# Performance work log

Measured on AMD Instinct MI355X. Metric: run time of the kernel, lower is better.

Reference implementation:

```python
import jax, jax.numpy as jnp
import numpy as np

B, S, DIM = 16, 1024, 1024
GAMMA = 0.96875
EPS = 1e-3  # keras GroupNormalization default epsilon


def setup_inputs() -> dict:
    key = jax.random.key(0)
    ks = jax.random.split(key, 4)
    scale = 1.0 / np.sqrt(DIM)
    return {
        "x": jax.random.normal(ks[0], (B, S, DIM), dtype=jnp.float32),
        "Wq": jax.random.normal(ks[1], (DIM, DIM), dtype=jnp.float32) * scale,
        "Wk": jax.random.normal(ks[2], (DIM, DIM), dtype=jnp.float32) * scale,
        "Wv": jax.random.normal(ks[3], (DIM, DIM), dtype=jnp.float32) * scale,
        "gn_scale": jnp.ones((DIM,), dtype=jnp.float32),
        "gn_beta": jnp.zeros((DIM,), dtype=jnp.float32),
    }


def reference(x, Wq, Wk, Wv, gn_scale, gn_beta):
    # Bias-free projections
    Q = x @ Wq  # [B,S,D]
    K = x @ Wk
    V = x @ Wv
    # Full (non-causal) exponential decay matrix D[i,j] = gamma^(i-j)
    idx = jnp.arange(S, dtype=jnp.float32)
    D = GAMMA ** (idx[:, None] - idx[None, :])  # [S,S]
    scores = jnp.einsum("bsd,btd->bst", Q, K) * D  # [B,S,S]
    y = scores @ V  # [B,S,D]
    # GroupNorm with groups == channels: normalize each channel over seq axis
    mean = jnp.mean(y, axis=1, keepdims=True)  # [B,1,D]
    var = jnp.var(y, axis=1, keepdims=True)
    y_hat = (y - mean) * jax.lax.rsqrt(var + EPS)
    return y_hat * gn_scale + gn_beta
```

## Files before the change

### kernel.cpp

```cpp
#include <hip/hip_runtime.h>
#include <cmath>

#define BATCH_ 16
#define SN_ 1024
#define DN_ 1024

constexpr float EPS_ = 1e-3f;

typedef unsigned short ushort;
typedef __attribute__((ext_vector_type(8))) short short8;
typedef __attribute__((ext_vector_type(8))) unsigned short ushort8;
typedef __attribute__((ext_vector_type(16))) float f32x16;

__device__ __forceinline__ ushort f2b(float f) {
    unsigned u = __float_as_uint(f);
    unsigned r = (u + 0x7fffu + ((u >> 16) & 1u)) >> 16;
    return (ushort)r;
}

__device__ __forceinline__ void gload16(const void* g, void* l) {
    __builtin_amdgcn_global_load_lds(
        (const __attribute__((address_space(1))) void*)g,
        (__attribute__((address_space(3))) void*)l, 16, 0, 0);
}

template<int MODE>
__global__ __launch_bounds__(512, 2)
void gemm_bf(const ushort* __restrict__ A0, const ushort* __restrict__ B0,
             void* __restrict__ C0, long sA, long sB, long sBm, long sC,
             float coef)
{
    constexpr bool TRANSP = (MODE == 2 || MODE == 3);
    constexpr bool SCALE  = (MODE == 1 || MODE == 3);

    __shared__ __align__(16) char lds[131072];

    const int gx = gridDim.x, gy = gridDim.y;
    int lid   = blockIdx.x + gx * (blockIdx.y + gy * blockIdx.z);
    int total = gx * gy * gridDim.z;
    int swz   = (lid & 7) * (total >> 3) + (lid >> 3);
    int bx = swz % gx;
    int rest = swz / gx;
    int by = rest % gy;
    int bz = rest / gy;

    const int m0 = by * 256, n0 = bx * 256;
    const ushort* A  = A0 + (long)bz * sA;
    const ushort* Bp = B0 + (long)bz * sB + (long)(m0 >> 10) * sBm;

    const int t = threadIdx.x;
    const int l = t & 63, w = t >> 6;
    const int wr = w >> 2, wc = w & 3;
    const int ln = l & 31;
    const int kb = l >> 5;
    const int lx = l & 7;

    const int aOff = (wr * 128 + ln) * 128;
    const int bOff = 32768 + (wc * 64 + ln) * 128;

    const int rl   = t >> 3;
    const int slot = (t & 7) ^ (rl & 7);
    const ushort* gA = A  + (long)(m0 + rl) * 1024 + slot * 8;
    const ushort* gB = Bp + (long)(n0 + rl) * 1024 + slot * 8;
    char* lA = lds + t * 16;
    char* lB = lds + 32768 + t * 16;

    f32x16 acc[4][2] = {};

#pragma unroll
    for (int h = 0; h < 4; ++h) {
        gload16(gA + (long)h * 64 * 1024, lA + h * 8192);
        gload16(gB + (long)h * 64 * 1024, lB + h * 8192);
    }
    __syncthreads();

    int buf = 0;
    for (int kt = 0; kt < 16; ++kt) {
        if (kt < 15) {
            int k0 = (kt + 1) * 64;
            int bo = (buf ^ 1) * 65536;
#pragma unroll
            for (int h = 0; h < 4; ++h) {
                gload16(gA + (long)h * 64 * 1024 + k0, lA + bo + h * 8192);
                gload16(gB + (long)h * 64 * 1024 + k0, lB + bo + h * 8192);
            }
        }
        const int bo = buf * 65536;
#pragma unroll
        for (int ks = 0; ks < 4; ++ks) {
            const int sx = ((ks * 2 + kb) ^ lx) * 16;
            short8 av[4], bv[2];
#pragma unroll
            for (int mi = 0; mi < 4; ++mi)
                av[mi] = *(const short8*)(lds + bo + aOff + mi * 4096 + sx);
#pragma unroll
            for (int nj = 0; nj < 2; ++nj)
                bv[nj] = *(const short8*)(lds + bo + bOff + nj * 4096 + sx);
            __builtin_amdgcn_s_setprio(1);
#pragma unroll
            for (int mi = 0; mi < 4; ++mi)
#pragma unroll
                for (int nj = 0; nj < 2; ++nj)
                    acc[mi][nj] = __builtin_amdgcn_mfma_f32_32x32x16_bf16(
                        av[mi], bv[nj], acc[mi][nj], 0, 0, 0);
            __builtin_amdgcn_s_setprio(0);
        }
        __syncthreads();
        buf ^= 1;
    }

    if constexpr (MODE == 0) {
        float* C = (float*)C0 + (long)bz * sC;
#pragma unroll
        for (int mi = 0; mi < 4; ++mi)
#pragma unroll
            for (int reg = 0; reg < 16; ++reg) {
                int row = m0 + wr * 128 + mi * 32 + (reg & 3) + 8 * (reg >> 2) + 4 * kb;
#pragma unroll
                for (int nj = 0; nj < 2; ++nj)
                    C[(long)row * 1024 + n0 + wc * 64 + nj * 32 + ln] =
                        acc[mi][nj][reg];
            }
    } else if constexpr (!TRANSP) {
        ushort* C = (ushort*)C0 + (long)bz * sC;
#pragma unroll
        for (int mi = 0; mi < 4; ++mi)
#pragma unroll
            for (int reg = 0; reg < 16; ++reg) {
                int row = m0 + wr * 128 + mi * 32 + (reg & 3) + 8 * (reg >> 2) + 4 * kb;
                float s = SCALE ? exp2f(coef * (float)(row & 1023)) : 1.0f;
#pragma unroll
                for (int nj = 0; nj < 2; ++nj)
                    C[(long)row * 1024 + n0 + wc * 64 + nj * 32 + ln] =
                        f2b(acc[mi][nj][reg] * s);
            }
    } else {
        ushort* Tl = (ushort*)lds;
        const int bb = m0 >> 10;
        const int ms = m0 & 1023;
        ushort* Ct = (ushort*)C0 + (long)bb * sC;
#pragma unroll
        for (int mi = 0; mi < 4; ++mi)
#pragma unroll
            for (int reg = 0; reg < 16; ++reg) {
                int rm = wr * 128 + mi * 32 + (reg & 3) + 8 * (reg >> 2) + 4 * kb;
                float s = SCALE ? exp2f(coef * (float)(ms + rm)) : 1.0f;
#pragma unroll
                for (int nj = 0; nj < 2; ++nj) {
                    int cn = wc * 64 + nj * 32 + ln;
                    int p  = (rm >> 3) ^ (cn & 31);
                    Tl[cn * 256 + p * 8 + (rm & 7)] = f2b(acc[mi][nj][reg] * s);
                }
            }
        __syncthreads();
#pragma unroll
        for (int it = 0; it < 16; ++it) {
            int cn = (t >> 5) + it * 16;
            int ch = t & 31;
            int p  = ch ^ (cn & 31);
            ushort8 v = *(const ushort8*)&Tl[cn * 256 + p * 8];
            *(ushort8*)&Ct[(long)(n0 + cn) * 1024 + ms + ch * 8] = v;
        }
    }
}

__global__ __launch_bounds__(256)
void conv_x_k(const float* __restrict__ x, ushort* __restrict__ xb)
{
    long i = ((long)blockIdx.x * 256 + threadIdx.x) * 8;
    float4 a = *(const float4*)&x[i];
    float4 b = *(const float4*)&x[i + 4];
    ushort8 v;
    v[0] = f2b(a.x); v[1] = f2b(a.y); v[2] = f2b(a.z); v[3] = f2b(a.w);
    v[4] = f2b(b.x); v[5] = f2b(b.y); v[6] = f2b(b.z); v[7] = f2b(b.w);
    *(ushort8*)&xb[i] = v;
}

__global__ __launch_bounds__(256)
void wt_k(const float* __restrict__ W, ushort* __restrict__ Wt)
{
    __shared__ float Tl[32][33];
    int tx = threadIdx.x & 31, ty = threadIdx.x >> 5;
    int c0 = blockIdx.x * 32, r0 = blockIdx.y * 32;
#pragma unroll
    for (int i = 0; i < 4; i++)
        Tl[ty + 8 * i][tx] = W[(long)(r0 + ty + 8 * i) * 1024 + c0 + tx];
    __syncthreads();
#pragma unroll
    for (int i = 0; i < 4; i++)
        Wt[(long)(c0 + ty + 8 * i) * 1024 + r0 + tx] = f2b(Tl[tx][ty + 8 * i]);
}

__global__ __launch_bounds__(256)
void stats1(const float* __restrict__ y, float* __restrict__ psum,
            float* __restrict__ psumsq)
{
    int d = blockIdx.x * 256 + threadIdx.x;
    int b = blockIdx.y;
    int z = blockIdx.z;
    const float* p = y + ((long)b * SN_ + (long)z * 128) * DN_ + d;
    float s = 0.f, ss = 0.f;
    for (int i = 0; i < 128; i++) {
        float v = p[(long)i * DN_];
        s += v;
        ss += v * v;
    }
    long o = ((long)z * BATCH_ + b) * DN_ + d;
    psum[o] = s;
    psumsq[o] = ss;
}

__global__ __launch_bounds__(256)
void stats2(const float* __restrict__ psum, const float* __restrict__ psumsq,
            const float* __restrict__ gsc, const float* __restrict__ gbt,
            float* __restrict__ fs, float* __restrict__ bias)
{
    int d = blockIdx.x * 256 + threadIdx.x;
    int b = blockIdx.y;
    float s = 0.f, ss = 0.f;
    for (int z = 0; z < 8; z++) {
        long o = ((long)z * BATCH_ + b) * DN_ + d;
        s += psum[o];
        ss += psumsq[o];
    }
    float mean = s * (1.0f / SN_);
    float var  = ss * (1.0f / SN_) - mean * mean;
    var = fmaxf(var, 0.0f);
    float rstd = rsqrtf(var + EPS_);
    float f = rstd * gsc[d];
    fs[(long)b * DN_ + d]   = f;
    bias[(long)b * DN_ + d] = gbt[d] - mean * f;
}

__global__ __launch_bounds__(256)
void norm_k(float* __restrict__ y, const float* __restrict__ fs,
            const float* __restrict__ bias)
{
    long i4 = (long)blockIdx.x * 256 + threadIdx.x;
    long e  = i4 * 4;
    int d = (int)(e & (DN_ - 1));
    int b = (int)(e >> 20);
    float4 v = *(float4*)&y[e];
    long o = (long)b * DN_ + d;
    float4 f  = *(const float4*)&fs[o];
    float4 bb = *(const float4*)&bias[o];
    v.x = v.x * f.x + bb.x;
    v.y = v.y * f.y + bb.y;
    v.z = v.z * f.z + bb.z;
    v.w = v.w * f.w + bb.w;
    *(float4*)&y[e] = v;
}

extern "C" void kernel_launch(void* const* d_in, const int* in_sizes, int n_in,
                              void* d_out, int out_size, void* d_ws, size_t ws_size,
                              hipStream_t stream)
{
    const float* x   = (const float*)d_in[0];
    const float* Wq  = (const float*)d_in[1];
    const float* Wk  = (const float*)d_in[2];
    const float* Wv  = (const float*)d_in[3];
    const float* gsc = (const float*)d_in[4];
    const float* gbt = (const float*)d_in[5];
    float* out = (float*)d_out;

    const long SD = (long)SN_ * DN_;
    const long DD = (long)DN_ * DN_;
    const size_t MB32 = (size_t)SD * BATCH_ * sizeof(ushort);

    char* ws = (char*)d_ws;
    ushort* xb  = (ushort*)(ws);
    ushort* Qp  = (ushort*)(ws + 1 * MB32);
    ushort* Kt  = (ushort*)(ws + 2 * MB32);
    ushort* Vt  = (ushort*)(ws + 3 * MB32);
    ushort* Mt  = (ushort*)(ws + 4 * MB32);
    ushort* Wtq = (ushort*)(ws + 5 * MB32);
    ushort* Wtk = (ushort*)(ws + 5 * MB32 + (2u << 20));
    ushort* Wtv = (ushort*)(ws + 5 * MB32 + (4u << 20));
    float*  psum   = (float*)(ws + 5 * MB32 + (6u << 20));
    float*  psumsq = (float*)(ws + 5 * MB32 + (6u << 20) + (1u << 19));
    float*  fs     = (float*)(ws + 5 * MB32 + (7u << 20));
    float*  bias   = (float*)(ws + 5 * MB32 + (7u << 20) + (1u << 18));

    const float lgf = (float)log2(0.96875);

    dim3 blk512(512);
    dim3 blk(256);
    dim3 gproj(4, 64);
    dim3 gmt(4, 4, 16);
    dim3 gy(4, 64);

    conv_x_k<<<dim3(8192), blk, 0, stream>>>(x, xb);
    wt_k<<<dim3(32, 32), blk, 0, stream>>>(Wq, Wtq);
    wt_k<<<dim3(32, 32), blk, 0, stream>>>(Wk, Wtk);
    wt_k<<<dim3(32, 32), blk, 0, stream>>>(Wv, Wtv);

    gemm_bf<1><<<gproj, blk512, 0, stream>>>(xb, Wtq, Qp, 0, 0, 0, 0, lgf);
    gemm_bf<3><<<gproj, blk512, 0, stream>>>(xb, Wtk, Kt, 0, 0, 0, SD, -lgf);
    gemm_bf<2><<<gproj, blk512, 0, stream>>>(xb, Wtv, Vt, 0, 0, 0, SD, 0.0f);
    gemm_bf<4><<<gmt, blk512, 0, stream>>>(Vt, Kt, Mt, SD, SD, 0, DD, 0.0f);
    gemm_bf<0><<<gy, blk512, 0, stream>>>(Qp, Mt, out, 0, 0, DD, 0, 0.0f);

    stats1<<<dim3(4, 16, 8), blk, 0, stream>>>(out, psum, psumsq);
    stats2<<<dim3(4, 16), blk, 0, stream>>>(psum, psumsq, gsc, gbt, fs, bias);
    norm_k<<<dim3(16384), blk, 0, stream>>>(out, fs, bias);
}
```

Before: 263.5 us.

## Interleave global-to-LDS prefetch with MFMA phases in GEMM main loop

Restructures the bf16 GEMM main loop into four phases, one per M sub-tile. Each phase loads its A fragments, issues part of the next K-tile's global_load_lds, and then runs its MFMAs, with explicit sched_barriers, s_barriers and partial vmcnt waits in place of a full __syncthreads per iteration. The goal is to overlap global memory traffic with matrix math and avoid draining all loads at the end of each iteration. In exchange it adds more barriers per iteration and depends on hand-tuned vmcnt counts, which makes the correctness of the LDS buffer handoff fragile. A __syncthreads is added before the transpose epilogue reuses LDS.

```diff
diff --git a/kernel.cpp b/kernel.cpp
--- a/kernel.cpp
+++ b/kernel.cpp
@@ -23,6 +23,9 @@
         (const __attribute__((address_space(1))) void*)g,
         (__attribute__((address_space(3))) void*)l, 16, 0, 0);
 }
+
+#define SCHED0 __builtin_amdgcn_sched_barrier(0)
+#define CFENCE asm volatile("" ::: "memory")
 
 template<int MODE>
 __global__ __launch_bounds__(512, 2)
@@ -57,6 +60,9 @@
 
     const int aOff = (wr * 128 + ln) * 128;
     const int bOff = 32768 + (wc * 64 + ln) * 128;
+    int sx[4];
+#pragma unroll
+    for (int ks = 0; ks < 4; ++ks) sx[ks] = (((ks * 2) + kb) ^ lx) * 16;
 
     const int rl   = t >> 3;
     const int slot = (t & 7) ^ (rl & 7);
@@ -65,48 +71,111 @@
     char* lA = lds + t * 16;
     char* lB = lds + 32768 + t * 16;
 
+#define STA(h, k0, bo_) gload16(gA + (long)(h) * 65536 + (k0), lA + (bo_) + (h) * 8192)
+#define STB(h, k0, bo_) gload16(gB + (long)(h) * 65536 + (k0), lB + (bo_) + (h) * 8192)
+
     f32x16 acc[4][2] = {};
 
-#pragma unroll
-    for (int h = 0; h < 4; ++h) {
-        gload16(gA + (long)h * 64 * 1024, lA + h * 8192);
-        gload16(gB + (long)h * 64 * 1024, lB + h * 8192);
-    }
-    __syncthreads();
-
-    int buf = 0;
+    STB(0, 0, 0); STB(1, 0, 0); STB(2, 0, 0); STB(3, 0, 0);
+    STA(0, 0, 0); STA(2, 0, 0); STA(1, 0, 0); STA(3, 0, 0);
+    SCHED0;
+    asm volatile("s_waitcnt vmcnt(2)" ::: "memory");
+    __builtin_amdgcn_s_barrier();
+    CFENCE; SCHED0;
+
     for (int kt = 0; kt < 16; ++kt) {
-        if (kt < 15) {
-            int k0 = (kt + 1) * 64;
-            int bo = (buf ^ 1) * 65536;
-#pragma unroll
-            for (int h = 0; h < 4; ++h) {
-                gload16(gA + (long)h * 64 * 1024 + k0, lA + bo + h * 8192);
-                gload16(gB + (long)h * 64 * 1024 + k0, lB + bo + h * 8192);
-            }
-        }
-        const int bo = buf * 65536;
-#pragma unroll
-        for (int ks = 0; ks < 4; ++ks) {
-            const int sx = ((ks * 2 + kb) ^ lx) * 16;
-            short8 av[4], bv[2];
-#pragma unroll
-            for (int mi = 0; mi < 4; ++mi)
-                av[mi] = *(const short8*)(lds + bo + aOff + mi * 4096 + sx);
-#pragma unroll
-            for (int nj = 0; nj < 2; ++nj)
-                bv[nj] = *(const short8*)(lds + bo + bOff + nj * 4096 + sx);
-            __builtin_amdgcn_s_setprio(1);
-#pragma unroll
-            for (int mi = 0; mi < 4; ++mi)
-#pragma unroll
-                for (int nj = 0; nj < 2; ++nj)
-                    acc[mi][nj] = __builtin_amdgcn_mfma_f32_32x32x16_bf16(
-                        av[mi], bv[nj], acc[mi][nj], 0, 0, 0);
-            __builtin_amdgcn_s_setprio(0);
-        }
-        __syncthreads();
-        buf ^= 1;
+        const int bo = (kt & 1) << 16;
+        const int bn = bo ^ 65536;
+        const int k1 = (kt + 1) << 6;
+        const bool st = kt < 15;
+
+        short8 bv[2][4], av[4];
+
+#pragma unroll
+        for (int ks = 0; ks < 4; ++ks) {
+            bv[0][ks] = *(const short8*)(lds + bo + bOff + 0 * 4096 + sx[ks]);
+            bv[1][ks] = *(const short8*)(lds + bo + bOff + 1 * 4096 + sx[ks]);
+            av[ks]    = *(const short8*)(lds + bo + aOff + 0 * 4096 + sx[ks]);
+        }
+        if (st) { STB(0, k1, bn); STB(1, k1, bn); }
+        SCHED0;
+        __builtin_amdgcn_s_barrier();
+        CFENCE; SCHED0;
+        __builtin_amdgcn_s_setprio(1);
+#pragma unroll
+        for (int ks = 0; ks < 4; ++ks) {
+            acc[0][0] = __builtin_amdgcn_mfma_f32_32x32x16_bf16(
+                av[ks], bv[0][ks], acc[0][0], 0, 0, 0);
+            acc[0][1] = __builtin_amdgcn_mfma_f32_32x32x16_bf16(
+                av[ks], bv[1][ks], acc[0][1], 0, 0, 0);
+        }
+        __builtin_amdgcn_s_setprio(0);
+        SCHED0;
+        __builtin_amdgcn_s_barrier();
+        CFENCE; SCHED0;
+
+#pragma unroll
+        for (int ks = 0; ks < 4; ++ks)
+            av[ks] = *(const short8*)(lds + bo + aOff + 1 * 4096 + sx[ks]);
+        if (st) { STB(2, k1, bn); STB(3, k1, bn); }
+        SCHED0;
+        __builtin_amdgcn_s_barrier();
+        CFENCE; SCHED0;
+        __builtin_amdgcn_s_setprio(1);
+#pragma unroll
+        for (int ks = 0; ks < 4; ++ks) {
+            acc[1][0] = __builtin_amdgcn_mfma_f32_32x32x16_bf16(
+                av[ks], bv[0][ks], acc[1][0], 0, 0, 0);
+            acc[1][1] = __builtin_amdgcn_mfma_f32_32x32x16_bf16(
+                av[ks], bv[1][ks], acc[1][1], 0, 0, 0);
+        }
+        __builtin_amdgcn_s_setprio(0);
+        SCHED0;
+        if (kt == 15) asm volatile("s_waitcnt vmcnt(0)" ::: "memory");
+        else          asm volatile("s_waitcnt vmcnt(4)" ::: "memory");
+        __builtin_amdgcn_s_barrier();
+        CFENCE; SCHED0;
+
+#pragma unroll
+        for (int ks = 0; ks < 4; ++ks)
+            av[ks] = *(const short8*)(lds + bo + aOff + 2 * 4096 + sx[ks]);
+        if (st) { STA(0, k1, bn); STA(2, k1, bn); }
+        SCHED0;
+        __builtin_amdgcn_s_barrier();
+        CFENCE; SCHED0;
+        __builtin_amdgcn_s_setprio(1);
+#pragma unroll
+        for (int ks = 0; ks < 4; ++ks) {
+            acc[2][0] = __builtin_amdgcn_mfma_f32_32x32x16_bf16(
+                av[ks], bv[0][ks], acc[2][0], 0, 0, 0);
+            acc[2][1] = __builtin_amdgcn_mfma_f32_32x32x16_bf16(
+                av[ks], bv[1][ks], acc[2][1], 0, 0, 0);
+        }
+        __builtin_amdgcn_s_setprio(0);
+        SCHED0;
+        __builtin_amdgcn_s_barrier();
+        CFENCE; SCHED0;
+
+#pragma unroll
+        for (int ks = 0; ks < 4; ++ks)
+            av[ks] = *(const short8*)(lds + bo + aOff + 3 * 4096 + sx[ks]);
+        if (st) { STA(1, k1, bn); STA(3, k1, bn); }
+        SCHED0;
+        __builtin_amdgcn_s_barrier();
+        CFENCE; SCHED0;
+        __builtin_amdgcn_s_setprio(1);
+#pragma unroll
+        for (int ks = 0; ks < 4; ++ks) {
+            acc[3][0] = __builtin_amdgcn_mfma_f32_32x32x16_bf16(
+                av[ks], bv[0][ks], acc[3][0], 0, 0, 0);
+            acc[3][1] = __builtin_amdgcn_mfma_f32_32x32x16_bf16(
+                av[ks], bv[1][ks], acc[3][1], 0, 0, 0);
+        }
+        __builtin_amdgcn_s_setprio(0);
+        SCHED0;
+        asm volatile("s_waitcnt vmcnt(2)" ::: "memory");
+        __builtin_amdgcn_s_barrier();
+        CFENCE; SCHED0;
     }
 
     if constexpr (MODE == 0) {
@@ -139,6 +208,7 @@
         const int bb = m0 >> 10;
         const int ms = m0 & 1023;
         ushort* Ct = (ushort*)C0 + (long)bb * sC;
+        __syncthreads();
 #pragma unroll
         for (int mi = 0; mi < 4; ++mi)
 #pragma unroll
@@ -162,6 +232,8 @@
             *(ushort8*)&Ct[(long)(n0 + cn) * 1024 + ms + ch * 8] = v;
         }
     }
+#undef STA
+#undef STB
 }
 
 __global__ __launch_bounds__(256)
```

Measured after the change: 261.1 us. Within noise of the previous version (-0.9%).
